# Optimization experiments

Measured on AMD Instinct MI355X. Metric: run time of the kernel, lower is better.

Reference implementation:

```python
import jax, jax.numpy as jnp
import numpy as np

# Module hyperparameters (from init_kwargs)
H, W = 256, 256
NUM_ANGLE, NUM_RHO = 360, 360
MASK_WIDTH = 3.0
N, C = 16, 1


def setup_inputs() -> dict:
    key = jax.random.key(0)
    hough_map = jax.random.uniform(key, (N, C, NUM_ANGLE, NUM_RHO), dtype=jnp.float32)
    return {"hough_map": hough_map}


def _peak_mask(hough_map):
    # max_pool2d(k=3, s=1, p=1) local-max detection + 0.5*global-max threshold
    pooled = jax.lax.reduce_window(
        hough_map, -jnp.inf, jax.lax.max,
        window_dimensions=(1, 1, 3, 3), window_strides=(1, 1, 1, 1), padding="SAME")
    gmax = jnp.max(hough_map, axis=(-2, -1), keepdims=True)
    return (hough_map == pooled) & (hough_map > 0.5 * gmax)


def reference(hough_map):
    n, c, A, R = hough_map.shape
    peak = _peak_mask(hough_map).astype(jnp.float32)  # [N,C,A,R], 0/1

    # xy grid centered at image center (matches torch meshgrid indexing='ij')
    yv = jnp.arange(H, dtype=jnp.float32) - (H - 1) / 2
    xv = jnp.arange(W, dtype=jnp.float32) - (W - 1) / 2
    yy, xx = jnp.meshgrid(yv, xv, indexing="ij")
    xflat, yflat = xx.ravel(), yy.ravel()  # [H*W]

    delta_rho = 2.0 * float(np.sqrt((W / 2) ** 2 + (H / 2) ** 2)) / (NUM_RHO - 1)
    rho_vals = (jnp.arange(R, dtype=jnp.float32) - R / 2) * delta_rho  # [R]
    thetas = jnp.arange(A, dtype=jnp.float32) * (np.pi / NUM_ANGLE)    # [A]
    cos_t, sin_t = jnp.cos(thetas), jnp.sin(thetas)

    # Per (n,c): out = any over peaks (a,r) of |cos_a*x + sin_a*y - rho_r| < w.
    # Since peak/line masks are 0/1, max-over-peaks == (boolean matmul > 0).
    # Scan over angles to avoid materializing the [A,R,H*W] line tensor.
    peak_per_a = peak.reshape(n * c, A, R).transpose(1, 0, 2)  # [A, NC, R]

    def body(carry, inp):
        ct, st, pk = inp                       # pk: [NC, R]
        rho_cal = ct * xflat + st * yflat      # [HW]
        line = (jnp.abs(rho_cal[None, :] - rho_vals[:, None]) < MASK_WIDTH)
        hit = pk @ line.astype(jnp.float32)    # [NC, HW]
        return jnp.maximum(carry, jnp.where(hit > 0, 1.0, 0.0)), None

    init = jnp.zeros((n * c, H * W), jnp.float32)
    out, _ = jax.lax.scan(body, init, (cos_t, sin_t, peak_per_a))
    return out.reshape(n, c, H, W)
```

## Files before the change

kernel.cpp:

```cpp
#include <hip/hip_runtime.h>
#include <math.h>

#define NN 16
#define AA 360
#define RR 360
#define HH 256
#define WW 256
#define WORDS 7
#define BAND 8
#define NBAND (AA / BAND)
#define NBLK (NN * NBAND)
#define PTHR 384
#define CAP 16
#define OTHR 512

__device__ __forceinline__ bool fhit(float rc, int r, float drho) {
    const float rho = __fmul_rn((float)(r - 180), drho);
    return fabsf(__fsub_rn(rc, rho)) < 3.0f;
}

__global__ void __launch_bounds__(PTHR)
k_peaks(const float* __restrict__ h, float* __restrict__ part,
        float* __restrict__ tab, unsigned long long* __restrict__ bits,
        uint2* __restrict__ lowlist, float dtheta) {
    __shared__ float rows[BAND + 2][RR];
    __shared__ float s_red[6];
    __shared__ int s_cnt;
    const int blk  = blockIdx.x;
    const int n    = blk / NBAND;
    const int band = blk % NBAND;
    const int a0   = band * BAND;
    const int t    = threadIdx.x;

    if (t == 0) s_cnt = 0;

    if (a0 > 0 && a0 + BAND < AA) {
        const float4* src = (const float4*)(h + ((size_t)n * AA + a0 - 1) * RR);
        float4* dst = (float4*)&rows[0][0];
        for (int i = t; i < (BAND + 2) * RR / 4; i += PTHR) dst[i] = src[i];
    } else {
        for (int i = t; i < (BAND + 2) * RR; i += PTHR) {
            const int aa = a0 - 1 + i / RR;
            (&rows[0][0])[i] = (aa >= 0 && aa < AA)
                ? h[((size_t)n * AA + aa) * RR + (i - (i / RR) * RR)] : -INFINITY;
        }
    }
    if (blk == 0) {
        for (int a = t; a < AA; a += PTHR) {
            float th = __fmul_rn((float)a, dtheta);
            tab[a]      = (float)cos((double)th);
            tab[AA + a] = (float)sin((double)th);
        }
    }
    __syncthreads();

    {
        const float* cen = &rows[1][0];
        float m = 0.0f;
        for (int i = t; i < BAND * RR; i += PTHR) m = fmaxf(m, cen[i]);
        #pragma unroll
        for (int s = 32; s > 0; s >>= 1) m = fmaxf(m, __shfl_down(m, s, 64));
        if ((t & 63) == 0) s_red[t >> 6] = m;
        __syncthreads();
        if (t == 0) {
            m = s_red[0];
            #pragma unroll
            for (int i = 1; i < 6; ++i) m = fmaxf(m, s_red[i]);
            part[blk] = m;
        }
    }

    const int r = t;
    float hm[BAND + 2];
    if (r < RR) {
        #pragma unroll
        for (int j = 0; j < BAND + 2; ++j) {
            const float a_ = (r > 0)      ? rows[j][r - 1] : -INFINITY;
            const float c_ = (r < RR - 1) ? rows[j][r + 1] : -INFINITY;
            hm[j] = fmaxf(fmaxf(a_, rows[j][r]), c_);
        }
    }
    #pragma unroll
    for (int k = 0; k < BAND; ++k) {
        bool hi = false;
        if (r < RR) {
            const float v = rows[k + 1][r];
            const float pooled = fmaxf(fmaxf(hm[k], hm[k + 1]), hm[k + 2]);
            if (v >= pooled) {
                if (v >= 0.5f) hi = true;
                else {
                    const int slot = atomicAdd(&s_cnt, 1);
                    if (slot < CAP)
                        lowlist[blk * CAP + slot] =
                            make_uint2(((unsigned)(a0 + k) << 16) | (unsigned)r,
                                       __float_as_uint(v));
                }
            }
        }
        const unsigned long long m = __ballot(hi);
        if ((t & 63) == 0)
            bits[((size_t)n * AA + a0 + k) * WORDS + (t >> 6)] = m;
    }
    if (t < BAND)
        bits[((size_t)n * AA + a0 + t) * WORDS + 6] = 0ull;
    __syncthreads();
    for (int i = s_cnt + t; i < CAP; i += PTHR)
        lowlist[blk * CAP + i] = make_uint2(0u, 0u);
}

__global__ void __launch_bounds__(OTHR)
k_out(const unsigned long long* __restrict__ bits, const float* __restrict__ part,
      const float* __restrict__ tab, const uint2* __restrict__ lowlist,
      float* __restrict__ out, float inv_dr, float drho) {
    __shared__ __align__(16) unsigned long long Lb[AA * WORDS];
    __shared__ float Lct[AA], Lst[AA];
    __shared__ float s_gth;
    const int n     = blockIdx.x >> 6;
    const int chunk = blockIdx.x & 63;
    const int t     = threadIdx.x;

    if (t < 64) {
        float m = (t < NBAND) ? part[n * NBAND + t] : 0.0f;
        #pragma unroll
        for (int s = 32; s > 0; s >>= 1) m = fmaxf(m, __shfl_down(m, s, 64));
        if (t == 0) s_gth = 0.5f * m;
    }
    {
        const uint4* src = (const uint4*)(bits + (size_t)n * AA * WORDS);
        uint4* dst = (uint4*)Lb;
        for (int i = t; i < AA * WORDS / 2; i += OTHR) dst[i] = src[i];
        for (int i = t; i < AA; i += OTHR) {
            Lct[i] = tab[i];
            Lst[i] = tab[AA + i];
        }
    }
    __syncthreads();
    const float gth = s_gth;

    for (int i = t; i < NBAND * CAP; i += OTHR) {
        const uint2 e = lowlist[(size_t)n * NBAND * CAP + i];
        if (__uint_as_float(e.y) > gth) {
            const int a = e.x >> 16, rr = e.x & 0xffff;
            atomicOr((unsigned int*)Lb + a * (WORDS * 2) + (rr >> 5), 1u << (rr & 31));
        }
    }
    __syncthreads();

    const int pbase = chunk * 1024 + t;
    #pragma unroll
    for (int q = 0; q < 2; ++q) {
        const int p = pbase + q * OTHR;
        const int y = p >> 8;
        const int x = p & 255;
        const float xf = (float)x - 127.5f;
        const float yf = (float)y - 127.5f;
        float res = 0.0f;
        for (int a = 0; a < AA; ++a) {
            const float rc = __fadd_rn(__fmul_rn(Lct[a], xf), __fmul_rn(Lst[a], yf));
            const int lo_est = (int)ceilf (__fmul_rn(__fsub_rn(rc, 3.0f), inv_dr)) + 180;
            const int hi_est = (int)floorf(__fmul_rn(__fadd_rn(rc, 3.0f), inv_dr)) + 180;
            int lo = fhit(rc, lo_est - 1, drho) ? lo_est - 1
                   : (fhit(rc, lo_est, drho) ? lo_est : lo_est + 1);
            int hi = fhit(rc, hi_est + 1, drho) ? hi_est + 1
                   : (fhit(rc, hi_est, drho) ? hi_est : hi_est - 1);
            lo = lo < 0 ? 0 : lo;
            hi = hi > RR - 1 ? RR - 1 : hi;
            if (lo <= hi) {
                const int len = hi - lo + 1;
                const unsigned long long pmask = (1ull << len) - 1ull;
                const int sh = lo & 63;
                const int w  = lo >> 6;
                const unsigned long long m0 = pmask << sh;
                const unsigned long long m1 = sh ? (pmask >> (64 - sh)) : 0ull;
                const unsigned long long v0 = Lb[a * WORDS + w];
                const unsigned long long v1 = Lb[a * WORDS + w + 1];
                if ((v0 & m0) | (v1 & m1)) { res = 1.0f; break; }
            }
        }
        out[(size_t)n * (HH * WW) + p] = res;
    }
}

extern "C" void kernel_launch(void* const* d_in, const int* in_sizes, int n_in,
                              void* d_out, int out_size, void* d_ws, size_t ws_size,
                              hipStream_t stream) {
    const float* h = (const float*)d_in[0];
    float* out = (float*)d_out;

    char* ws = (char*)d_ws;
    unsigned long long* bits = (unsigned long long*)ws;
    float* part = (float*)(ws + (size_t)NN * AA * WORDS * 8);
    float* tab  = part + NBLK;
    uint2* lowlist = (uint2*)(tab + 2 * AA);

    const double dr_d = 2.0 * sqrt((WW / 2.0) * (WW / 2.0) + (HH / 2.0) * (HH / 2.0)) / (RR - 1);
    const float drho   = (float)dr_d;
    const float inv_dr = (float)(1.0 / dr_d);
    const float dtheta = (float)(3.14159265358979323846 / 360.0);

    k_peaks<<<NBLK, PTHR, 0, stream>>>(h, part, tab, bits, lowlist, dtheta);
    k_out<<<NN * 64, OTHR, 0, stream>>>(bits, part, tab, lowlist, out, inv_dr, drho);
}
```

Baseline: 72.61 us.

## Tile output pixels in 8x8 blocks and test rho windows with 32-bit shifted bitmasks

The per-angle peak bitmaps are stored with an 8-bit offset in 32-bit words, so a rho window is pulled out with a single 64-bit shift instead of 64-bit mask pairs and boundary fhit searches. Exact boundary checks now run only on the edge bits. Each wavefront handles an 8x8 pixel tile, so neighbouring pixels tend to exit early together, and results are staged through shared memory for coalesced stores. Computing the cos/sin table is spread across many blocks and packed as float2. The gain is less divergence and fewer ALU operations, at the cost of more complex bit logic and an extra shared-memory staging step.

```diff
diff --git a/kernel.cpp b/kernel.cpp
--- a/kernel.cpp
+++ b/kernel.cpp
@@ -6,7 +6,8 @@
 #define RR 360
 #define HH 256
 #define WW 256
-#define WORDS 7
+#define W64 8
+#define W32 16
 #define BAND 8
 #define NBAND (AA / BAND)
 #define NBLK (NN * NBAND)
@@ -21,9 +22,10 @@
 
 __global__ void __launch_bounds__(PTHR)
 k_peaks(const float* __restrict__ h, float* __restrict__ part,
-        float* __restrict__ tab, unsigned long long* __restrict__ bits,
+        float2* __restrict__ tab2, unsigned long long* __restrict__ bits,
         uint2* __restrict__ lowlist, float dtheta) {
     __shared__ float rows[BAND + 2][RR];
+    __shared__ unsigned long long sball[BAND][6];
     __shared__ float s_red[6];
     __shared__ int s_cnt;
     const int blk  = blockIdx.x;
@@ -45,12 +47,9 @@
                 ? h[((size_t)n * AA + aa) * RR + (i - (i / RR) * RR)] : -INFINITY;
         }
     }
-    if (blk == 0) {
-        for (int a = t; a < AA; a += PTHR) {
-            float th = __fmul_rn((float)a, dtheta);
-            tab[a]      = (float)cos((double)th);
-            tab[AA + a] = (float)sin((double)th);
-        }
+    if (blk < AA && t == 0) {
+        const float th = __fmul_rn((float)blk, dtheta);
+        tab2[blk] = make_float2((float)cos((double)th), (float)sin((double)th));
     }
     __syncthreads();
 
@@ -98,22 +97,27 @@
             }
         }
         const unsigned long long m = __ballot(hi);
-        if ((t & 63) == 0)
-            bits[((size_t)n * AA + a0 + k) * WORDS + (t >> 6)] = m;
-    }
-    if (t < BAND)
-        bits[((size_t)n * AA + a0 + t) * WORDS + 6] = 0ull;
-    __syncthreads();
+        if ((t & 63) == 0) sball[k][t >> 6] = m;
+    }
+    __syncthreads();
+
+    if (t < BAND * W64) {
+        const int k = t >> 3, j = t & 7;
+        const unsigned long long bj = (j < 6) ? sball[k][j] : 0ull;
+        const unsigned long long bm = (j >= 1 && j <= 6) ? sball[k][j - 1] : 0ull;
+        bits[((size_t)n * AA + a0 + k) * W64 + j] = (bj << 8) | (bm >> 56);
+    }
     for (int i = s_cnt + t; i < CAP; i += PTHR)
         lowlist[blk * CAP + i] = make_uint2(0u, 0u);
 }
 
 __global__ void __launch_bounds__(OTHR)
 k_out(const unsigned long long* __restrict__ bits, const float* __restrict__ part,
-      const float* __restrict__ tab, const uint2* __restrict__ lowlist,
+      const float2* __restrict__ tab2, const uint2* __restrict__ lowlist,
       float* __restrict__ out, float inv_dr, float drho) {
-    __shared__ __align__(16) unsigned long long Lb[AA * WORDS];
-    __shared__ float Lct[AA], Lst[AA];
+    __shared__ __align__(16) unsigned int Lw[AA * W32];
+    __shared__ float2 Lcs[AA];
+    __shared__ float sres[32 * 32];
     __shared__ float s_gth;
     const int n     = blockIdx.x >> 6;
     const int chunk = blockIdx.x & 63;
@@ -126,13 +130,10 @@
         if (t == 0) s_gth = 0.5f * m;
     }
     {
-        const uint4* src = (const uint4*)(bits + (size_t)n * AA * WORDS);
-        uint4* dst = (uint4*)Lb;
-        for (int i = t; i < AA * WORDS / 2; i += OTHR) dst[i] = src[i];
-        for (int i = t; i < AA; i += OTHR) {
-            Lct[i] = tab[i];
-            Lst[i] = tab[AA + i];
-        }
+        const uint4* src = (const uint4*)(bits + (size_t)n * AA * W64);
+        uint4* dst = (uint4*)Lw;
+        for (int i = t; i < AA * W32 / 4; i += OTHR) dst[i] = src[i];
+        for (int i = t; i < AA; i += OTHR) Lcs[i] = tab2[i];
     }
     __syncthreads();
     const float gth = s_gth;
@@ -141,43 +142,58 @@
         const uint2 e = lowlist[(size_t)n * NBAND * CAP + i];
         if (__uint_as_float(e.y) > gth) {
             const int a = e.x >> 16, rr = e.x & 0xffff;
-            atomicOr((unsigned int*)Lb + a * (WORDS * 2) + (rr >> 5), 1u << (rr & 31));
-        }
-    }
-    __syncthreads();
-
-    const int pbase = chunk * 1024 + t;
-    #pragma unroll
+            const int p = rr + 8;
+            atomicOr(&Lw[a * W32 + (p >> 5)], 1u << (p & 31));
+        }
+    }
+    __syncthreads();
+
+    const int Oy = (chunk >> 3) << 5;
+    const int Ox = (chunk & 7) << 5;
+    const int wv = t >> 6;
+    const int l  = t & 63;
+    const int ly = l >> 3, lx = l & 7;
+
     for (int q = 0; q < 2; ++q) {
-        const int p = pbase + q * OTHR;
-        const int y = p >> 8;
-        const int x = p & 255;
-        const float xf = (float)x - 127.5f;
-        const float yf = (float)y - 127.5f;
+        const int sub = wv * 2 + q;
+        const int py  = ((sub >> 2) << 3) + ly;
+        const int px  = ((sub & 3) << 3) + lx;
+        const float xf = (float)(Ox + px) - 127.5f;
+        const float yf = (float)(Oy + py) - 127.5f;
         float res = 0.0f;
-        for (int a = 0; a < AA; ++a) {
-            const float rc = __fadd_rn(__fmul_rn(Lct[a], xf), __fmul_rn(Lst[a], yf));
+        int abase = 0;
+        for (int a = 0; a < AA; ++a, abase += W32) {
+            const float2 cs = Lcs[a];
+            const float rc = __fadd_rn(__fmul_rn(cs.x, xf), __fmul_rn(cs.y, yf));
             const int lo_est = (int)ceilf (__fmul_rn(__fsub_rn(rc, 3.0f), inv_dr)) + 180;
             const int hi_est = (int)floorf(__fmul_rn(__fadd_rn(rc, 3.0f), inv_dr)) + 180;
-            int lo = fhit(rc, lo_est - 1, drho) ? lo_est - 1
-                   : (fhit(rc, lo_est, drho) ? lo_est : lo_est + 1);
-            int hi = fhit(rc, hi_est + 1, drho) ? hi_est + 1
-                   : (fhit(rc, hi_est, drho) ? hi_est : hi_est - 1);
-            lo = lo < 0 ? 0 : lo;
-            hi = hi > RR - 1 ? RR - 1 : hi;
-            if (lo <= hi) {
-                const int len = hi - lo + 1;
-                const unsigned long long pmask = (1ull << len) - 1ull;
-                const int sh = lo & 63;
-                const int w  = lo >> 6;
-                const unsigned long long m0 = pmask << sh;
-                const unsigned long long m1 = sh ? (pmask >> (64 - sh)) : 0ull;
-                const unsigned long long v0 = Lb[a * WORDS + w];
-                const unsigned long long v1 = Lb[a * WORDS + w + 1];
-                if ((v0 & m0) | (v1 & m1)) { res = 1.0f; break; }
+            const int Lo  = lo_est + 7;
+            const int len = hi_est - lo_est + 3;
+            const int w   = Lo >> 5;
+            const unsigned lo32 = Lw[abase + w];
+            const unsigned hi32 = Lw[abase + w + 1];
+            const int sh = Lo & 31;
+            const unsigned win = (unsigned)(((((unsigned long long)hi32) << 32) | lo32) >> sh);
+            const unsigned m   = (1u << len) - 1u;
+            const unsigned bw  = win & m;
+            if (bw == 0u) continue;
+            const unsigned innerM = (m >> 4) << 2;
+            if (bw & innerM) { res = 1.0f; break; }
+            unsigned e = bw & ~innerM;
+            bool hit = false;
+            while (e) {
+                const int b = __ffs(e) - 1; e &= e - 1;
+                if (fhit(rc, lo_est - 1 + b, drho)) { hit = true; break; }
             }
-        }
-        out[(size_t)n * (HH * WW) + p] = res;
+            if (hit) { res = 1.0f; break; }
+        }
+        sres[py * 32 + px] = res;
+    }
+    __syncthreads();
+    for (int q = 0; q < 2; ++q) {
+        const int idx = q * OTHR + t;
+        out[(size_t)n * (HH * WW) + (size_t)(Oy + (idx >> 5)) * WW + Ox + (idx & 31)]
+            = sres[idx];
     }
 }
 
@@ -189,15 +205,15 @@
 
     char* ws = (char*)d_ws;
     unsigned long long* bits = (unsigned long long*)ws;
-    float* part = (float*)(ws + (size_t)NN * AA * WORDS * 8);
-    float* tab  = part + NBLK;
-    uint2* lowlist = (uint2*)(tab + 2 * AA);
+    float*  part    = (float*)(ws + (size_t)NN * AA * W64 * 8);
+    float2* tab2    = (float2*)(part + NBLK);
+    uint2*  lowlist = (uint2*)((char*)tab2 + AA * sizeof(float2));
 
     const double dr_d = 2.0 * sqrt((WW / 2.0) * (WW / 2.0) + (HH / 2.0) * (HH / 2.0)) / (RR - 1);
     const float drho   = (float)dr_d;
     const float inv_dr = (float)(1.0 / dr_d);
     const float dtheta = (float)(3.14159265358979323846 / 360.0);
 
-    k_peaks<<<NBLK, PTHR, 0, stream>>>(h, part, tab, bits, lowlist, dtheta);
-    k_out<<<NN * 64, OTHR, 0, stream>>>(bits, part, tab, lowlist, out, inv_dr, drho);
-}
+    k_peaks<<<NBLK, PTHR, 0, stream>>>(h, part, tab2, bits, lowlist, dtheta);
+    k_out<<<NN * 64, OTHR, 0, stream>>>(bits, part, tab2, lowlist, out, inv_dr, drho);
+}
```

After: 70.07 us. -3.5%, faster.
